# Kernel tuning notes

Hardware: AMD Instinct MI355X
Metric: run time of the kernel (lower is better)

The kernel has to match this reference:

```python
import jax, jax.numpy as jnp
import numpy as np

B, T, H, D = 2, 2048, 8, 128
HID = H * D          # 1024
K_CONV = 4
EPS = 1e-5


def causal_dwconv(x, w, b):
    # x: [B,T,C], w: [C,K], b: [C]
    # torch Conv1d(groups=C, padding=K-1) followed by [..., :T] == left-padded causal depthwise conv
    K = w.shape[1]
    Tx = x.shape[1]
    xp = jnp.pad(x, ((0, 0), (K - 1, 0), (0, 0)))
    acc = jnp.zeros_like(x)
    for j in range(K):  # tiny fixed loop over kernel taps
        acc = acc + xp[:, j:j + Tx, :] * w[:, j]
    return acc + b


def setup_inputs() -> dict:
    key = jax.random.key(0)
    ks = jax.random.split(key, 16)
    s = 0.02
    inp = {
        'x':   jax.random.normal(ks[0], (B, T, HID), jnp.float32),
        'Wq':  s * jax.random.normal(ks[1], (HID, H * D), jnp.float32),
        'Wk':  s * jax.random.normal(ks[2], (HID, H * D), jnp.float32),
        'Wv':  s * jax.random.normal(ks[3], (HID, H * D), jnp.float32),
        'Wa':  s * jax.random.normal(ks[4], (HID, H * D), jnp.float32),
        'ba':  jnp.zeros((H * D,), jnp.float32),
        'Wb':  s * jax.random.normal(ks[5], (HID, H), jnp.float32),
        'bb':  jnp.zeros((H,), jnp.float32),
        'Wg':  s * jax.random.normal(ks[6], (HID, H * D), jnp.float32),
        'Wo':  s * jax.random.normal(ks[7], (H * D, HID), jnp.float32),
        'cqw': s * jax.random.normal(ks[8], (H * D, K_CONV), jnp.float32),
        'cqb': jnp.zeros((H * D,), jnp.float32),
        'ckw': s * jax.random.normal(ks[9], (H * D, K_CONV), jnp.float32),
        'ckb': jnp.zeros((H * D,), jnp.float32),
        'cvw': s * jax.random.normal(ks[10], (H * D, K_CONV), jnp.float32),
        'cvb': jnp.zeros((H * D,), jnp.float32),
        'ln_g': jnp.ones((D,), jnp.float32),
        'ln_b': jnp.zeros((D,), jnp.float32),
    }
    return inp


def reference(x, Wq, Wk, Wv, Wa, ba, Wb, bb, Wg, Wo,
              cqw, cqb, ckw, ckb, cvw, cvb, ln_g, ln_b):
    Bx, Tx, _ = x.shape
    q = x @ Wq
    k = x @ Wk
    v = x @ Wv
    q = jax.nn.silu(causal_dwconv(q, cqw, cqb))
    k = jax.nn.silu(causal_dwconv(k, ckw, ckb))
    v = jax.nn.silu(causal_dwconv(v, cvw, cvb))
    q = q.reshape(Bx, Tx, H, D)
    k = k.reshape(Bx, Tx, H, D) * (D ** -0.5)   # k scaled by head_dim_qk**-0.5
    v = v.reshape(Bx, Tx, H, D)
    a = jax.nn.sigmoid(x @ Wa + ba).reshape(Bx, Tx, H, D)
    beta = jax.nn.sigmoid(x @ Wb + bb)           # [B,T,H]

    # delta-rule recurrent scan; state S: [B,H,Dv,Dk]
    def step(S, inp):
        q_t, k_t, v_t, a_t, b_t = inp            # [B,H,D] / beta [B,H]
        delta = jnp.einsum('bhvk,bhk->bhv', S, k_t)
        err = delta - v_t
        S = a_t[..., None] * S - (b_t[..., None] * err)[..., None] * k_t[:, :, None, :]
        o_t = jnp.einsum('bhvk,bhk->bhv', S, q_t)
        return S, o_t

    tfirst = lambda z: jnp.moveaxis(z, 1, 0)     # [B,T,...] -> [T,B,...]
    S0 = jnp.zeros((Bx, H, D, D), x.dtype)
    _, o = jax.lax.scan(step, S0, (tfirst(q), tfirst(k), tfirst(v), tfirst(a), tfirst(beta)))
    o = jnp.moveaxis(o, 0, 1)                    # [B,T,H,D]

    # LayerNorm over head_dim_v
    mu = o.mean(-1, keepdims=True)
    var = ((o - mu) ** 2).mean(-1, keepdims=True)
    o = (o - mu) * jax.lax.rsqrt(var + EPS) * ln_g + ln_b

    g = jax.nn.sigmoid(x @ Wg).reshape(Bx, Tx, H, D)
    o = (o * g).reshape(Bx, Tx, H * D)
    return o @ Wo
```

## Files before the change

kernel.cpp:

```cpp
#include <hip/hip_runtime.h>
#include <hip/hip_bf16.h>
#include <cstdint>
#include <cstddef>

#define BATCH 2
#define TLEN  2048
#define NHEAD 8
#define HD    128
#define HIDN  1024
#define MTOT  4096
#define MAT_ELEMS 1048576
#define XELEMS 4194304

typedef _Float16 f16;
typedef _Float16 f16x2 __attribute__((ext_vector_type(2)));
typedef _Float16 f16x8 __attribute__((ext_vector_type(8)));
typedef float    f32x4 __attribute__((ext_vector_type(4)));

__device__ __forceinline__ float sigmoidf_(float v) { return 1.0f / (1.0f + __expf(-v)); }

__device__ __forceinline__ float fdot2_(f16x2 a, f16x2 b, float c)
{
#if __has_builtin(__builtin_amdgcn_fdot2)
    return __builtin_amdgcn_fdot2(a, b, c, false);
#else
    return fmaf((float)a.x, (float)b.x, fmaf((float)a.y, (float)b.y, c));
#endif
}

__global__ __launch_bounds__(256) void convert_x_kernel(const float* __restrict__ x,
                                                        f16* __restrict__ x16)
{
    int i = (blockIdx.x * 256 + threadIdx.x) * 4;
    float4 v = *(const float4*)(x + i);
    union { f16 h[4]; uint2 u; } pk;
    pk.h[0] = (f16)v.x; pk.h[1] = (f16)v.y; pk.h[2] = (f16)v.z; pk.h[3] = (f16)v.w;
    *(uint2*)(x16 + i) = pk.u;
}

__global__ __launch_bounds__(256) void transpose_convert_kernel(
    const float* __restrict__ Wq, const float* __restrict__ Wk, const float* __restrict__ Wv,
    const float* __restrict__ Wa, const float* __restrict__ Wg, const float* __restrict__ Wo,
    f16* __restrict__ WT)
{
    __shared__ float tile[32][33];
    int mat = blockIdx.z;
    const float* W = (mat == 0) ? Wq : (mat == 1) ? Wk : (mat == 2) ? Wv
                   : (mat == 3) ? Wa : (mat == 4) ? Wg : Wo;
    int k0 = blockIdx.y * 32, n0 = blockIdx.x * 32;
    int tr = threadIdx.x >> 3;
    int tc = (threadIdx.x & 7) * 4;
    float4 vin = *(const float4*)(W + (size_t)(k0 + tr) * HIDN + n0 + tc);
    tile[tr][tc + 0] = vin.x; tile[tr][tc + 1] = vin.y;
    tile[tr][tc + 2] = vin.z; tile[tr][tc + 3] = vin.w;
    __syncthreads();
    f16* dst = WT + (size_t)(mat * HIDN + n0 + tr) * HIDN + k0 + tc;
    union { f16 h[4]; uint2 u; } pk;
    pk.h[0] = (f16)tile[tc + 0][tr]; pk.h[1] = (f16)tile[tc + 1][tr];
    pk.h[2] = (f16)tile[tc + 2][tr]; pk.h[3] = (f16)tile[tc + 3][tr];
    *(uint2*)dst = pk.u;
}

template <int MODE>
__global__ __launch_bounds__(256) void gemm_f16(
    const f16* __restrict__ A, const f16* __restrict__ BT,
    float* __restrict__ out_f32,
    f16* __restrict__ qkv_hat, float* __restrict__ a_buf, f16* __restrict__ g16,
    const float* __restrict__ ba)
{
    __shared__ __align__(16) f16 As[128][40];
    __shared__ __align__(16) f16 Bs[128][40];
    int m0 = blockIdx.y * 128;
    int n0 = blockIdx.x * 128;
    int tid = threadIdx.x;
    int w = tid >> 6, lane = tid & 63;
    int L16 = lane & 15, quad = lane >> 4;
    int wm = (w >> 1) * 64, wn = (w & 1) * 64;

    f32x4 acc[4][4];
#pragma unroll
    for (int i = 0; i < 4; ++i)
#pragma unroll
        for (int j = 0; j < 4; ++j) acc[i][j] = (f32x4){0.f, 0.f, 0.f, 0.f};

    int ldr = tid >> 2;
    int ldc = (tid & 3) * 8;

    for (int k0 = 0; k0 < 1024; k0 += 32) {
        uint4 a0 = *(const uint4*)(A + (size_t)(m0 + ldr) * HIDN + k0 + ldc);
        uint4 a1 = *(const uint4*)(A + (size_t)(m0 + ldr + 64) * HIDN + k0 + ldc);
        uint4 b0 = *(const uint4*)(BT + (size_t)(n0 + ldr) * HIDN + k0 + ldc);
        uint4 b1 = *(const uint4*)(BT + (size_t)(n0 + ldr + 64) * HIDN + k0 + ldc);
        __syncthreads();
        *(uint4*)(&As[ldr][ldc]) = a0;
        *(uint4*)(&As[ldr + 64][ldc]) = a1;
        *(uint4*)(&Bs[ldr][ldc]) = b0;
        *(uint4*)(&Bs[ldr + 64][ldc]) = b1;
        __syncthreads();
        f16x8 af[4], bf[4];
#pragma unroll
        for (int i = 0; i < 4; ++i) {
            af[i] = *(const f16x8*)(&As[wm + i * 16 + L16][quad * 8]);
            bf[i] = *(const f16x8*)(&Bs[wn + i * 16 + L16][quad * 8]);
        }
#pragma unroll
        for (int i = 0; i < 4; ++i)
#pragma unroll
            for (int j = 0; j < 4; ++j)
                acc[i][j] = __builtin_amdgcn_mfma_f32_16x16x32_f16(af[i], bf[j], acc[i][j], 0, 0, 0);
    }

#pragma unroll
    for (int i = 0; i < 4; ++i) {
#pragma unroll
        for (int j = 0; j < 4; ++j) {
            f32x4 c = acc[i][j];
            int mbase = m0 + wm + i * 16 + quad * 4;
            int n = n0 + wn + j * 16 + L16;
            if (MODE == 1) {
#pragma unroll
                for (int r = 0; r < 4; ++r)
                    out_f32[(size_t)(mbase + r) * HIDN + n] = c[r];
            } else {
                int mat = n >> 10;
                int nn = n & 1023;
                if (mat < 3) {
#pragma unroll
                    for (int r = 0; r < 4; ++r)
                        qkv_hat[(size_t)mat * XELEMS + (size_t)(mbase + r) * HIDN + nn] = (f16)c[r];
                } else if (mat == 3) {
                    float bav = ba[nn];
#pragma unroll
                    for (int r = 0; r < 4; ++r)
                        a_buf[(size_t)(mbase + r) * HIDN + nn] = sigmoidf_(c[r] + bav);
                } else {
#pragma unroll
                    for (int r = 0; r < 4; ++r)
                        g16[(size_t)(mbase + r) * HIDN + nn] = (f16)sigmoidf_(c[r]);
                }
            }
        }
    }
}

__global__ __launch_bounds__(256) void beta_kernel(const float* __restrict__ x,
                                                   const float* __restrict__ Wb,
                                                   const float* __restrict__ bb,
                                                   float* __restrict__ beta_buf)
{
    int row = blockIdx.x;
    int h = threadIdx.x >> 5, lane = threadIdx.x & 31;
    const float* xr = x + (size_t)row * HIDN;
    float part = 0.f;
    for (int i = lane; i < HIDN; i += 32)
        part += xr[i] * Wb[i * NHEAD + h];
#pragma unroll
    for (int m = 1; m <= 16; m <<= 1) part += __shfl_xor(part, m);
    if (lane == 0)
        beta_buf[(size_t)row * NHEAD + h] = sigmoidf_(part + bb[h]);
}

__global__ __launch_bounds__(256) void conv_silu_kernel(
    const f16* __restrict__ qkv_hat,
    const float* __restrict__ cqw, const float* __restrict__ cqb,
    const float* __restrict__ ckw, const float* __restrict__ ckb,
    const float* __restrict__ cvw, const float* __restrict__ cvb,
    f16* __restrict__ qkv16)
{
    int z = blockIdx.y;
    int row = blockIdx.x;
    int tloc = row & (TLEN - 1);
    int c4 = threadIdx.x * 4;
    const f16* src = qkv_hat + (size_t)z * XELEMS;
    const float* w  = (z == 0) ? cqw : (z == 1) ? ckw : cvw;
    const float* bi = (z == 0) ? cqb : (z == 1) ? ckb : cvb;

    float xv[4][4];
#pragma unroll
    for (int j = 0; j < 4; ++j) {
        int tt = tloc - 3 + j;
        if (tt >= 0) {
            const f16* p = src + (size_t)(row - 3 + j) * HIDN + c4;
            xv[j][0] = (float)p[0]; xv[j][1] = (float)p[1];
            xv[j][2] = (float)p[2]; xv[j][3] = (float)p[3];
        } else {
            xv[j][0] = xv[j][1] = xv[j][2] = xv[j][3] = 0.f;
        }
    }
    float scale = (z == 1) ? 0.08838834764831845f : 1.0f;
    union { f16 h[4]; uint2 u; } pk;
#pragma unroll
    for (int cc = 0; cc < 4; ++cc) {
        float4 wc = *(const float4*)(w + (size_t)(c4 + cc) * 4);
        float acc = bi[c4 + cc] + wc.x * xv[0][cc] + wc.y * xv[1][cc]
                                 + wc.z * xv[2][cc] + wc.w * xv[3][cc];
        pk.h[cc] = (f16)(acc * sigmoidf_(acc) * scale);
    }
    *(uint2*)(qkv16 + (size_t)z * XELEMS + (size_t)row * HIDN + c4) = pk.u;
}

#define SCAN_C 32
#define SSC  1024.0f
#define ISSC 0.0009765625f

__global__ __launch_bounds__(64) void scan_kernel(
    const f16* __restrict__ q16, const f16* __restrict__ k16, const f16* __restrict__ v16,
    const float* __restrict__ a_buf, const float* __restrict__ beta_buf,
    float* __restrict__ o_buf)
{
    __shared__ __align__(16) float Sp[16 * 132];
    __shared__ __align__(16) f16   Sp16[16 * 136];
    __shared__ __align__(16) f16   Ks[32 * 136];
    __shared__ __align__(16) f16   Gf[32 * 40];
    __shared__ __align__(16) f16   Qf[32 * 40];
    __shared__ __align__(16) float skv[16 * 34];
    __shared__ __align__(16) float sqv[16 * 34];
    __shared__ __align__(16) float avb[16 * 68];
    __shared__ __align__(16) float Bts[32];
    __shared__ __align__(16) f16   c16s[16 * 40];
    __shared__ __align__(16) float PCs[16];

    int bh = blockIdx.x;
    int b = bh >> 3, h = bh & 7;
    int v0 = blockIdx.y * 16;
    int lane = threadIdx.x;
    int L16 = lane & 15, quad = lane >> 4;
    int vl = lane >> 2, li = lane & 3;
    int t_av = lane >> 1, halfsel = lane & 1;
    const size_t rowbase = (size_t)(b * TLEN) * HIDN + h * HD;

    f16x8 kf[2][4], qf[2][4];
    float4 ar0, ar1; uint4 vr; float betr = 0.f;

    auto prefetch = [&](int t0) {
#pragma unroll
        for (int nt = 0; nt < 2; ++nt)
#pragma unroll
            for (int kk = 0; kk < 4; ++kk) {
                size_t g = rowbase + (size_t)(t0 + nt * 16 + L16) * HIDN + kk * 32 + quad * 8;
                kf[nt][kk] = *(const f16x8*)(k16 + g);
                qf[nt][kk] = *(const f16x8*)(q16 + g);
            }
        size_t ga = rowbase + (size_t)(t0 + t_av) * HIDN + v0 + halfsel * 8;
        ar0 = *(const float4*)(a_buf + ga);
        ar1 = *(const float4*)(a_buf + ga + 4);
        vr  = *(const uint4*)(v16 + ga);
        betr = beta_buf[((size_t)(b * TLEN) + t0 + t_av) * NHEAD + h];
    };

    auto stage = [&]() {
#pragma unroll
        for (int nt = 0; nt < 2; ++nt)
#pragma unroll
            for (int kk = 0; kk < 4; ++kk)
                *(f16x8*)(&Ks[(nt * 16 + L16) * 136 + kk * 32 + quad * 8]) = kf[nt][kk];
        const f16* vh = (const f16*)&vr;
        const float* aa0 = (const float*)&ar0;
        const float* aa1 = (const float*)&ar1;
#pragma unroll
        for (int e = 0; e < 4; ++e) {
            float2 w; w.x = aa0[e]; w.y = betr * (float)vh[e];
            *(float2*)(&avb[(halfsel * 8 + e) * 68 + 2 * t_av]) = w;
        }
#pragma unroll
        for (int e = 0; e < 4; ++e) {
            float2 w; w.x = aa1[e]; w.y = betr * (float)vh[4 + e];
            *(float2*)(&avb[(halfsel * 8 + 4 + e) * 68 + 2 * t_av]) = w;
        }
        if (halfsel == 0) Bts[t_av] = betr;
    };

    auto computeMM = [&]() {
        f32x4 accG[2][2], accKQ[2][2], accK[2], accQ[2];
#pragma unroll
        for (int i = 0; i < 2; ++i) {
            accK[i] = (f32x4){0, 0, 0, 0}; accQ[i] = (f32x4){0, 0, 0, 0};
#pragma unroll
            for (int j = 0; j < 2; ++j) { accG[i][j] = (f32x4){0, 0, 0, 0}; accKQ[i][j] = (f32x4){0, 0, 0, 0}; }
        }
#pragma unroll
        for (int kk = 0; kk < 4; ++kk) {
            f16x8 sf = *(const f16x8*)(&Sp16[L16 * 136 + kk * 32 + quad * 8]);
#pragma unroll
            for (int nt = 0; nt < 2; ++nt) {
                accK[nt] = __builtin_amdgcn_mfma_f32_16x16x32_f16(sf, kf[nt][kk], accK[nt], 0, 0, 0);
                accQ[nt] = __builtin_amdgcn_mfma_f32_16x16x32_f16(sf, qf[nt][kk], accQ[nt], 0, 0, 0);
#pragma unroll
                for (int mt = 0; mt < 2; ++mt) {
                    accG[mt][nt]  = __builtin_amdgcn_mfma_f32_16x16x32_f16(kf[mt][kk], kf[nt][kk], accG[mt][nt], 0, 0, 0);
                    accKQ[mt][nt] = __builtin_amdgcn_mfma_f32_16x16x32_f16(kf[mt][kk], qf[nt][kk], accKQ[mt][nt], 0, 0, 0);
                }
            }
        }
#pragma unroll
        for (int nt = 0; nt < 2; ++nt) {
            int t = nt * 16 + L16;
#pragma unroll
            for (int mt = 0; mt < 2; ++mt) {
                union { f16 e[4]; uint2 u2; } pg, pq;
#pragma unroll
                for (int r = 0; r < 4; ++r) {
                    pg.e[r] = (f16)accG[mt][nt][r];
                    pq.e[r] = (f16)accKQ[mt][nt][r];
                }
                *(uint2*)(&Gf[t * 40 + mt * 16 + quad * 4]) = pg.u2;
                *(uint2*)(&Qf[t * 40 + mt * 16 + quad * 4]) = pq.u2;
            }
#pragma unroll
            for (int r = 0; r < 4; ++r) {
                skv[(quad * 4 + r) * 34 + t] = accK[nt][r];
                sqv[(quad * 4 + r) * 34 + t] = accQ[nt][r];
            }
        }
    };

    prefetch(0);
    for (int i = lane; i < 16 * 132; i += 64) Sp[i] = 0.f;
    for (int i = lane; i < 16 * 136; i += 64) Sp16[i] = (f16)0.f;

    const size_t obase = rowbase + v0 + vl;
    const int NCH = TLEN / SCAN_C;

    for (int ch = 0; ch < NCH; ++ch) {
        int t0 = ch * SCAN_C;
        stage();
        computeMM();

        f16x8 bu[8];
#pragma unroll
        for (int kt = 0; kt < 8; ++kt)
#pragma unroll
            for (int j = 0; j < 8; ++j)
                bu[kt][j] = Ks[(quad * 8 + j) * 136 + kt * 16 + L16];

        if (ch < NCH - 1) prefetch(t0 + SCAN_C);

        {
            f16x2 c0, c1, c2, c3;
            c0.x = (f16)0.f; c0.y = (f16)0.f; c1 = c0; c2 = c0; c3 = c0;
            float P = 1.f;
            union RowU { uint4 u4; f16x2 p[4]; };
#pragma unroll
            for (int t = 0; t < SCAN_C; t += 2) {
                RowU g0u, g1u, h0u, h1u;
                g0u.u4 = *(const uint4*)(&Gf[t * 40 + li * 8]);
                g1u.u4 = *(const uint4*)(&Gf[(t + 1) * 40 + li * 8]);
                h0u.u4 = *(const uint4*)(&Qf[t * 40 + li * 8]);
                h1u.u4 = *(const uint4*)(&Qf[(t + 1) * 40 + li * 8]);
                float2 skp = *(const float2*)(&skv[vl * 34 + t]);
                float2 sqp = *(const float2*)(&sqv[vl * 34 + t]);
                float4 ab4 = *(const float4*)(&avb[vl * 68 + 2 * t]);
                float2 btp = *(const float2*)(&Bts[t]);
                float kq00 = (float)Qf[t * 40 + t];
                f16x2 dq  = *(const f16x2*)(&Qf[(t + 1) * 40 + t]);
                float g01 = (float)Gf[(t + 1) * 40 + t];

                float pG  = fdot2_(c0, g0u.p[0], fdot2_(c1, g0u.p[1], 0.f))
                          + fdot2_(c2, g0u.p[2], fdot2_(c3, g0u.p[3], 0.f));
                float pG1 = fdot2_(c0, g1u.p[0], fdot2_(c1, g1u.p[1], 0.f))
                          + fdot2_(c2, g1u.p[2], fdot2_(c3, g1u.p[3], 0.f));
                float pO  = fdot2_(c0, h0u.p[0], fdot2_(c1, h0u.p[1], 0.f))
                          + fdot2_(c2, h0u.p[2], fdot2_(c3, h0u.p[3], 0.f));
                float pO1 = fdot2_(c0, h1u.p[0], fdot2_(c1, h1u.p[1], 0.f))
                          + fdot2_(c2, h1u.p[2], fdot2_(c3, h1u.p[3], 0.f));
                int tmp;
                tmp = __builtin_amdgcn_update_dpp(0, __float_as_int(pG),  0xB1, 0xF, 0xF, true); pG  += __int_as_float(tmp);
                tmp = __builtin_amdgcn_update_dpp(0, __float_as_int(pG1), 0xB1, 0xF, 0xF, true); pG1 += __int_as_float(tmp);
                tmp = __builtin_amdgcn_update_dpp(0, __float_as_int(pO),  0xB1, 0xF, 0xF, true); pO  += __int_as_float(tmp);
                tmp = __builtin_amdgcn_update_dpp(0, __float_as_int(pO1), 0xB1, 0xF, 0xF, true); pO1 += __int_as_float(tmp);
                tmp = __builtin_amdgcn_update_dpp(0, __float_as_int(pG),  0x4E, 0xF, 0xF, true); pG  += __int_as_float(tmp);
                tmp = __builtin_amdgcn_update_dpp(0, __float_as_int(pG1), 0x4E, 0xF, 0xF, true); pG1 += __int_as_float(tmp);
                tmp = __builtin_amdgcn_update_dpp(0, __float_as_int(pO),  0x4E, 0xF, 0xF, true); pO  += __int_as_float(tmp);
                tmp = __builtin_amdgcn_update_dpp(0, __float_as_int(pO1), 0x4E, 0xF, 0xF, true); pO1 += __int_as_float(tmp);

                float a0 = ab4.x, bv0 = ab4.y, a1 = ab4.z, bv1 = ab4.w;
                float bt0 = btp.x, bt1 = btp.y;
                float sk0 = skp.x * ISSC, sk1 = skp.y * ISSC;
                float sq0 = sqp.x * ISSC, sq1 = sqp.y * ISSC;
                float kq01 = (float)dq.x, kq11 = (float)dq.y;

                float x0 = fmaf(P, sk0, pG);
                float u0 = fmaf(-bt0, x0, bv0);
                float P0 = P * a0;
                float o0 = fmaf(a0, pO, u0 * kq00);
                o0 = fmaf(P0, sq0, o0);
                float accGv = fmaf(a0, pG1, u0 * g01);
                float x1 = fmaf(P0, sk1, accGv);
                float u1 = fmaf(-bt1, x1, bv1);
                float P1 = P0 * a1;
                float accOv = fmaf(a0, pO1, u0 * kq01);
                float o1 = fmaf(a1, accOv, u1 * kq11);
                o1 = fmaf(P1, sq1, o1);

                float aa = a0 * a1;
                f16 aah = (f16)aa;
                f16x2 aa2; aa2.x = aah; aa2.y = aah;
                c0 *= aa2; c1 *= aa2; c2 *= aa2; c3 *= aa2;
                if (li == (t >> 3)) {
                    f16x2 un; un.x = (f16)(u0 * a1); un.y = (f16)u1;
                    int p = (t & 7) >> 1;
                    if (p == 0) c0 = un; else if (p == 1) c1 = un;
                    else if (p == 2) c2 = un; else c3 = un;
                }
                P = P1;
                if (li == 0) {
                    o_buf[obase + (size_t)(t0 + t) * HIDN]     = o0;
                    o_buf[obase + (size_t)(t0 + t + 1) * HIDN] = o1;
                }
            }
            f16 s16 = (f16)SSC;
            f16x2 ss2; ss2.x = s16; ss2.y = s16;
            union { f16x2 p[4]; uint4 u4; } pc;
            pc.p[0] = c0 * ss2; pc.p[1] = c1 * ss2; pc.p[2] = c2 * ss2; pc.p[3] = c3 * ss2;
            *(uint4*)(&c16s[vl * 40 + li * 8]) = pc.u4;
            if (li == 0) PCs[vl] = P;
        }

        if (ch < NCH - 1) {
            f16x8 ca = *(const f16x8*)(&c16s[L16 * 40 + quad * 8]);
            float pc = PCs[L16];
#pragma unroll
            for (int kt = 0; kt < 8; ++kt) {
                f32x4 d = __builtin_amdgcn_mfma_f32_16x16x32_f16(bu[kt], ca, (f32x4){0, 0, 0, 0}, 0, 0, 0);
                int idx = L16 * 132 + kt * 16 + quad * 4;
                float4 s = *(const float4*)(&Sp[idx]);
                s.x = fmaf(pc, s.x, d[0]);
                s.y = fmaf(pc, s.y, d[1]);
                s.z = fmaf(pc, s.z, d[2]);
                s.w = fmaf(pc, s.w, d[3]);
                *(float4*)(&Sp[idx]) = s;
                union { f16 e[4]; uint2 u2; } ph;
                ph.e[0] = (f16)s.x; ph.e[1] = (f16)s.y;
                ph.e[2] = (f16)s.z; ph.e[3] = (f16)s.w;
                *(uint2*)(&Sp16[L16 * 136 + kt * 16 + quad * 4]) = ph.u2;
            }
        }
    }
}

__global__ __launch_bounds__(256) void ln_gate_kernel(
    const float* __restrict__ o_buf, const f16* __restrict__ g16,
    const float* __restrict__ lng, const float* __restrict__ lnb,
    f16* __restrict__ og16)
{
    int row = blockIdx.x;
    int h = threadIdx.x >> 5, lane = threadIdx.x & 31;
    size_t base = (size_t)row * HIDN + h * HD + lane * 4;
    float4 x = *(const float4*)(o_buf + base);
    float s  = x.x + x.y + x.z + x.w;
    float sq = x.x * x.x + x.y * x.y + x.z * x.z + x.w * x.w;
#pragma unroll
    for (int m = 1; m <= 16; m <<= 1) {
        s  += __shfl_xor(s, m);
        sq += __shfl_xor(sq, m);
    }
    float mu  = s * (1.0f / 128.0f);
    float var = sq * (1.0f / 128.0f) - mu * mu;
    float inv = 1.0f / sqrtf(var + 1e-5f);
    int d = lane * 4;
    const float* xp = (const float*)&x;
    union { f16 h4[4]; uint2 u; } pk;
#pragma unroll
    for (int j = 0; j < 4; ++j) {
        float on = (xp[j] - mu) * inv * lng[d + j] + lnb[d + j];
        pk.h4[j] = (f16)(on * (float)g16[base + j]);
    }
    *(uint2*)(og16 + base) = pk.u;
}

extern "C" void kernel_launch(void* const* d_in, const int* in_sizes, int n_in,
                              void* d_out, int out_size, void* d_ws, size_t ws_size,
                              hipStream_t stream)
{
    (void)in_sizes; (void)n_in; (void)out_size; (void)ws_size;
    const float* x   = (const float*)d_in[0];
    const float* Wq  = (const float*)d_in[1];
    const float* Wk  = (const float*)d_in[2];
    const float* Wv  = (const float*)d_in[3];
    const float* Wa  = (const float*)d_in[4];
    const float* ba  = (const float*)d_in[5];
    const float* Wb  = (const float*)d_in[6];
    const float* bb  = (const float*)d_in[7];
    const float* Wg  = (const float*)d_in[8];
    const float* Wo  = (const float*)d_in[9];
    const float* cqw = (const float*)d_in[10];
    const float* cqb = (const float*)d_in[11];
    const float* ckw = (const float*)d_in[12];
    const float* ckb = (const float*)d_in[13];
    const float* cvw = (const float*)d_in[14];
    const float* cvb = (const float*)d_in[15];
    const float* lng = (const float*)d_in[16];
    const float* lnb = (const float*)d_in[17];
    float* out = (float*)d_out;

    char* ws = (char*)d_ws;
    f16*   x16      = (f16*)(ws + 0);
    f16*   WT       = (f16*)(ws + 8388608);
    f16*   qkvh     = (f16*)(ws + 20971520);
    f16*   qkv16    = (f16*)(ws + 46137344);
    float* a_buf    = (float*)(ws + 96468992);
    f16*   g16      = (f16*)(ws + 113246208);
    float* beta_buf = (float*)(ws + 121634816);
    float* o_buf    = (float*)(ws + 121765888);
    f16*   og16     = (f16*)(ws + 138543104);

    convert_x_kernel<<<dim3(4096), dim3(256), 0, stream>>>(x, x16);
    transpose_convert_kernel<<<dim3(32, 32, 6), dim3(256), 0, stream>>>(Wq, Wk, Wv, Wa, Wg, Wo, WT);
    gemm_f16<0><<<dim3(40, 32), dim3(256), 0, stream>>>(x16, WT, nullptr, qkvh, a_buf, g16, ba);
    beta_kernel<<<dim3(4096), dim3(256), 0, stream>>>(x, Wb, bb, beta_buf);
    conv_silu_kernel<<<dim3(4096, 3), dim3(256), 0, stream>>>(qkvh, cqw, cqb, ckw, ckb, cvw, cvb, qkv16);
    scan_kernel<<<dim3(16, 8), dim3(64), 0, stream>>>(
        qkv16, qkv16 + XELEMS, qkv16 + 2 * (size_t)XELEMS, a_buf, beta_buf, o_buf);
    ln_gate_kernel<<<dim3(4096), dim3(256), 0, stream>>>(o_buf, g16, lng, lnb, og16);
    gemm_f16<1><<<dim3(8, 32), dim3(256), 0, stream>>>(og16, WT + 5 * (size_t)MAT_ELEMS, out,
                                                       nullptr, nullptr, nullptr, nullptr);
}
```

Before: 614.2 us.

## Precompute chunk Gram matrices in a parallel kernel and warp-specialize the scan

A new gram_kernel computes the per-chunk K·K^T and K·Q^T Gram matrices, plus cross-chunk Gram terms and a transposed K, in parallel across all chunks, and writes them to the workspace. The scan becomes a two-wave block: one wave prefetches those matrices, a/beta/v and next-chunk K/Q into double-buffered LDS and runs the state-update and S·K/S·Q MFMAs, while the other wave runs the serial intra-chunk recurrence. This takes Gram work off the serial critical path and overlaps loads and state updates with the recurrence. In exchange it adds extra global traffic, an extra launch, per-chunk block barriers and a more intricate cross-chunk correction scheme.

```diff
diff --git a/kernel.cpp b/kernel.cpp
--- a/kernel.cpp
+++ b/kernel.cpp
@@ -11,6 +11,10 @@
 #define MTOT  4096
 #define MAT_ELEMS 1048576
 #define XELEMS 4194304
+#define SCAN_C 32
+#define NCH    64
+#define SSC  1024.0f
+#define ISSC 0.0009765625f
 
 typedef _Float16 f16;
 typedef _Float16 f16x2 __attribute__((ext_vector_type(2)));
@@ -199,241 +203,390 @@
     *(uint2*)(qkv16 + (size_t)z * XELEMS + (size_t)row * HIDN + c4) = pk.u;
 }
 
-#define SCAN_C 32
-#define SSC  1024.0f
-#define ISSC 0.0009765625f
-
-__global__ __launch_bounds__(64) void scan_kernel(
+__global__ __launch_bounds__(64) void gram_kernel(
+    const f16* __restrict__ q16, const f16* __restrict__ k16,
+    f16* __restrict__ G_g, f16* __restrict__ KQ_g,
+    f16* __restrict__ Gx_g, f16* __restrict__ Qx_g, f16* __restrict__ KT_g)
+{
+    int ch = blockIdx.x;
+    int bh = blockIdx.y;
+    int b = bh >> 3, h = bh & 7;
+    int lane = threadIdx.x;
+    int L16 = lane & 15, quad = lane >> 4;
+    size_t rowbase = (size_t)(b * TLEN) * HIDN + h * HD;
+    int t0 = ch * SCAN_C;
+    bool hasNext = (ch + 1 < NCH);
+
+    union ZU { uint4 u; f16x8 v; };
+    ZU zz; zz.u = (uint4){0, 0, 0, 0};
+
+    f16x8 kc[2][4], qc[2][4], kn[2][4], qn[2][4];
+#pragma unroll
+    for (int nt = 0; nt < 2; ++nt)
+#pragma unroll
+        for (int kk = 0; kk < 4; ++kk) {
+            size_t g = rowbase + (size_t)(t0 + nt * 16 + L16) * HIDN + kk * 32 + quad * 8;
+            kc[nt][kk] = *(const f16x8*)(k16 + g);
+            qc[nt][kk] = *(const f16x8*)(q16 + g);
+            if (hasNext) {
+                kn[nt][kk] = *(const f16x8*)(k16 + g + (size_t)SCAN_C * HIDN);
+                qn[nt][kk] = *(const f16x8*)(q16 + g + (size_t)SCAN_C * HIDN);
+            } else {
+                kn[nt][kk] = zz.v; qn[nt][kk] = zz.v;
+            }
+        }
+
+    f32x4 aG[2][2], aKQ[2][2], aGx[2][2], aQx[2][2];
+#pragma unroll
+    for (int i = 0; i < 2; ++i)
+#pragma unroll
+        for (int j = 0; j < 2; ++j) {
+            aG[i][j] = (f32x4){0, 0, 0, 0}; aKQ[i][j] = (f32x4){0, 0, 0, 0};
+            aGx[i][j] = (f32x4){0, 0, 0, 0}; aQx[i][j] = (f32x4){0, 0, 0, 0};
+        }
+#pragma unroll
+    for (int kk = 0; kk < 4; ++kk)
+#pragma unroll
+        for (int mt = 0; mt < 2; ++mt)
+#pragma unroll
+            for (int nt = 0; nt < 2; ++nt) {
+                aG[mt][nt]  = __builtin_amdgcn_mfma_f32_16x16x32_f16(kc[mt][kk], kc[nt][kk], aG[mt][nt], 0, 0, 0);
+                aKQ[mt][nt] = __builtin_amdgcn_mfma_f32_16x16x32_f16(kc[mt][kk], qc[nt][kk], aKQ[mt][nt], 0, 0, 0);
+                aGx[mt][nt] = __builtin_amdgcn_mfma_f32_16x16x32_f16(kc[mt][kk], kn[nt][kk], aGx[mt][nt], 0, 0, 0);
+                aQx[mt][nt] = __builtin_amdgcn_mfma_f32_16x16x32_f16(kc[mt][kk], qn[nt][kk], aQx[mt][nt], 0, 0, 0);
+            }
+
+    size_t gb = ((size_t)bh * NCH + ch) * 1024;
+#pragma unroll
+    for (int nt = 0; nt < 2; ++nt) {
+        int t = nt * 16 + L16;
+#pragma unroll
+        for (int mt = 0; mt < 2; ++mt) {
+            union { f16 e[4]; uint2 u2; } pg, pq, px, py;
+#pragma unroll
+            for (int r = 0; r < 4; ++r) {
+                pg.e[r] = (f16)aG[mt][nt][r];
+                pq.e[r] = (f16)aKQ[mt][nt][r];
+                px.e[r] = (f16)aGx[mt][nt][r];
+                py.e[r] = (f16)aQx[mt][nt][r];
+            }
+            *(uint2*)(G_g  + gb + t * 32 + mt * 16 + quad * 4) = pg.u2;
+            *(uint2*)(KQ_g + gb + t * 32 + mt * 16 + quad * 4) = pq.u2;
+            *(uint2*)(Gx_g + gb + t * 32 + mt * 16 + quad * 4) = px.u2;
+            *(uint2*)(Qx_g + gb + t * 32 + mt * 16 + quad * 4) = py.u2;
+        }
+    }
+    size_t kb = ((size_t)bh * NCH + ch) * 4096;
+#pragma unroll
+    for (int nt = 0; nt < 2; ++nt) {
+        int t = nt * 16 + L16;
+#pragma unroll
+        for (int kk = 0; kk < 4; ++kk)
+#pragma unroll
+            for (int j = 0; j < 8; ++j) {
+                int k = kk * 32 + quad * 8 + j;
+                KT_g[kb + (size_t)k * 32 + t] = kc[nt][kk][j];
+            }
+    }
+}
+
+__global__ __launch_bounds__(128) void scan2_kernel(
     const f16* __restrict__ q16, const f16* __restrict__ k16, const f16* __restrict__ v16,
     const float* __restrict__ a_buf, const float* __restrict__ beta_buf,
+    const f16* __restrict__ G_g, const f16* __restrict__ KQ_g,
+    const f16* __restrict__ Gx_g, const f16* __restrict__ Qx_g, const f16* __restrict__ KT_g,
     float* __restrict__ o_buf)
 {
     __shared__ __align__(16) float Sp[16 * 132];
     __shared__ __align__(16) f16   Sp16[16 * 136];
-    __shared__ __align__(16) f16   Ks[32 * 136];
-    __shared__ __align__(16) f16   Gf[32 * 40];
-    __shared__ __align__(16) f16   Qf[32 * 40];
-    __shared__ __align__(16) float skv[16 * 34];
-    __shared__ __align__(16) float sqv[16 * 34];
-    __shared__ __align__(16) float avb[16 * 68];
-    __shared__ __align__(16) float Bts[32];
-    __shared__ __align__(16) f16   c16s[16 * 40];
-    __shared__ __align__(16) float PCs[16];
-
-    int bh = blockIdx.x;
-    int b = bh >> 3, h = bh & 7;
-    int v0 = blockIdx.y * 16;
-    int lane = threadIdx.x;
-    int L16 = lane & 15, quad = lane >> 4;
-    int vl = lane >> 2, li = lane & 3;
-    int t_av = lane >> 1, halfsel = lane & 1;
+    __shared__ __align__(16) f16   KT_lds[128 * 32];
+    __shared__ __align__(16) f16   G_lds[2][1024];
+    __shared__ __align__(16) f16   Q_lds[2][1024];
+    __shared__ __align__(16) f16   Gx_lds[2][1024];
+    __shared__ __align__(16) f16   Qx_lds[2][1024];
+    __shared__ __align__(16) float skv[2][16 * 34];
+    __shared__ __align__(16) float sqv[2][16 * 34];
+    __shared__ __align__(16) float avb[2][16 * 68];
+    __shared__ __align__(16) float Bts[2][32];
+    __shared__ __align__(16) f16   c16s[2][16 * 40];
+    __shared__ __align__(16) float PCs[2][16];
+
+    const int tid = threadIdx.x;
+    const int wid = tid >> 6;
+    const int lane = tid & 63;
+    const int L16 = lane & 15, quad = lane >> 4;
+    const int vl = lane >> 2, li = lane & 3;
+    const int t_av = lane >> 1, halfsel = lane & 1;
+
+    const int bh = blockIdx.x;
+    const int b = bh >> 3, h = bh & 7;
+    const int v0 = blockIdx.y * 16;
     const size_t rowbase = (size_t)(b * TLEN) * HIDN + h * HD;
-
-    f16x8 kf[2][4], qf[2][4];
-    float4 ar0, ar1; uint4 vr; float betr = 0.f;
-
-    auto prefetch = [&](int t0) {
-#pragma unroll
-        for (int nt = 0; nt < 2; ++nt)
-#pragma unroll
-            for (int kk = 0; kk < 4; ++kk) {
-                size_t g = rowbase + (size_t)(t0 + nt * 16 + L16) * HIDN + kk * 32 + quad * 8;
-                kf[nt][kk] = *(const f16x8*)(k16 + g);
-                qf[nt][kk] = *(const f16x8*)(q16 + g);
-            }
-        size_t ga = rowbase + (size_t)(t0 + t_av) * HIDN + v0 + halfsel * 8;
-        ar0 = *(const float4*)(a_buf + ga);
-        ar1 = *(const float4*)(a_buf + ga + 4);
-        vr  = *(const uint4*)(v16 + ga);
-        betr = beta_buf[((size_t)(b * TLEN) + t0 + t_av) * NHEAD + h];
-    };
-
-    auto stage = [&]() {
-#pragma unroll
-        for (int nt = 0; nt < 2; ++nt)
-#pragma unroll
-            for (int kk = 0; kk < 4; ++kk)
-                *(f16x8*)(&Ks[(nt * 16 + L16) * 136 + kk * 32 + quad * 8]) = kf[nt][kk];
-        const f16* vh = (const f16*)&vr;
-        const float* aa0 = (const float*)&ar0;
-        const float* aa1 = (const float*)&ar1;
-#pragma unroll
-        for (int e = 0; e < 4; ++e) {
-            float2 w; w.x = aa0[e]; w.y = betr * (float)vh[e];
-            *(float2*)(&avb[(halfsel * 8 + e) * 68 + 2 * t_av]) = w;
-        }
-#pragma unroll
-        for (int e = 0; e < 4; ++e) {
-            float2 w; w.x = aa1[e]; w.y = betr * (float)vh[4 + e];
-            *(float2*)(&avb[(halfsel * 8 + 4 + e) * 68 + 2 * t_av]) = w;
-        }
-        if (halfsel == 0) Bts[t_av] = betr;
-    };
-
-    auto computeMM = [&]() {
-        f32x4 accG[2][2], accKQ[2][2], accK[2], accQ[2];
-#pragma unroll
-        for (int i = 0; i < 2; ++i) {
-            accK[i] = (f32x4){0, 0, 0, 0}; accQ[i] = (f32x4){0, 0, 0, 0};
-#pragma unroll
-            for (int j = 0; j < 2; ++j) { accG[i][j] = (f32x4){0, 0, 0, 0}; accKQ[i][j] = (f32x4){0, 0, 0, 0}; }
-        }
-#pragma unroll
-        for (int kk = 0; kk < 4; ++kk) {
-            f16x8 sf = *(const f16x8*)(&Sp16[L16 * 136 + kk * 32 + quad * 8]);
-#pragma unroll
-            for (int nt = 0; nt < 2; ++nt) {
-                accK[nt] = __builtin_amdgcn_mfma_f32_16x16x32_f16(sf, kf[nt][kk], accK[nt], 0, 0, 0);
-                accQ[nt] = __builtin_amdgcn_mfma_f32_16x16x32_f16(sf, qf[nt][kk], accQ[nt], 0, 0, 0);
-#pragma unroll
-                for (int mt = 0; mt < 2; ++mt) {
-                    accG[mt][nt]  = __builtin_amdgcn_mfma_f32_16x16x32_f16(kf[mt][kk], kf[nt][kk], accG[mt][nt], 0, 0, 0);
-                    accKQ[mt][nt] = __builtin_amdgcn_mfma_f32_16x16x32_f16(kf[mt][kk], qf[nt][kk], accKQ[mt][nt], 0, 0, 0);
-                }
-            }
-        }
-#pragma unroll
-        for (int nt = 0; nt < 2; ++nt) {
-            int t = nt * 16 + L16;
-#pragma unroll
-            for (int mt = 0; mt < 2; ++mt) {
-                union { f16 e[4]; uint2 u2; } pg, pq;
+    const size_t gmatbase = (size_t)bh * NCH;
+
+    {
+        for (int i = tid; i < 16 * 132; i += 128) Sp[i] = 0.f;
+        uint32_t* z;
+        z = (uint32_t*)Sp16;    for (int i = tid; i < 16 * 136 / 2; i += 128) z[i] = 0u;
+        z = (uint32_t*)KT_lds;  for (int i = tid; i < 128 * 32 / 2;  i += 128) z[i] = 0u;
+        z = (uint32_t*)G_lds;   for (int i = tid; i < 1024;          i += 128) z[i] = 0u;
+        z = (uint32_t*)Q_lds;   for (int i = tid; i < 1024;          i += 128) z[i] = 0u;
+        z = (uint32_t*)Gx_lds;  for (int i = tid; i < 1024;          i += 128) z[i] = 0u;
+        z = (uint32_t*)Qx_lds;  for (int i = tid; i < 1024;          i += 128) z[i] = 0u;
+        z = (uint32_t*)skv;     for (int i = tid; i < 2 * 16 * 34;   i += 128) z[i] = 0u;
+        z = (uint32_t*)sqv;     for (int i = tid; i < 2 * 16 * 34;   i += 128) z[i] = 0u;
+        z = (uint32_t*)avb;     for (int i = tid; i < 2 * 16 * 68;   i += 128) z[i] = 0u;
+        z = (uint32_t*)Bts;     for (int i = tid; i < 2 * 32;        i += 128) z[i] = 0u;
+        z = (uint32_t*)c16s;    for (int i = tid; i < 2 * 16 * 40 / 2; i += 128) z[i] = 0u;
+        z = (uint32_t*)PCs;     for (int i = tid; i < 2 * 16;        i += 128) z[i] = 0u;
+    }
+    __syncthreads();
+
+    if (wid == 1) {
+        f16x8 kf[2][4], qf[2][4];
+
+        {
+            size_t gb0 = gmatbase * 1024;
+            *(uint4*)(&G_lds[0][lane * 16])     = *(const uint4*)(G_g  + gb0 + lane * 16);
+            *(uint4*)(&G_lds[0][lane * 16 + 8]) = *(const uint4*)(G_g  + gb0 + lane * 16 + 8);
+            *(uint4*)(&Q_lds[0][lane * 16])     = *(const uint4*)(KQ_g + gb0 + lane * 16);
+            *(uint4*)(&Q_lds[0][lane * 16 + 8]) = *(const uint4*)(KQ_g + gb0 + lane * 16 + 8);
+            size_t ga = rowbase + (size_t)t_av * HIDN + v0 + halfsel * 8;
+            float4 ar0 = *(const float4*)(a_buf + ga);
+            float4 ar1 = *(const float4*)(a_buf + ga + 4);
+            uint4  vr  = *(const uint4*)(v16 + ga);
+            float betr = beta_buf[((size_t)(b * TLEN) + t_av) * NHEAD + h];
+            const f16* vh = (const f16*)&vr;
+            const float* aa0 = (const float*)&ar0;
+            const float* aa1 = (const float*)&ar1;
+#pragma unroll
+            for (int e = 0; e < 4; ++e) {
+                float2 wv; wv.x = aa0[e]; wv.y = betr * (float)vh[e];
+                *(float2*)(&avb[0][(halfsel * 8 + e) * 68 + 2 * t_av]) = wv;
+                float2 wu; wu.x = aa1[e]; wu.y = betr * (float)vh[4 + e];
+                *(float2*)(&avb[0][(halfsel * 8 + 4 + e) * 68 + 2 * t_av]) = wu;
+            }
+            if (halfsel == 0) Bts[0][t_av] = betr;
+        }
+        __syncthreads();
+
+        for (int ch = 0; ch < NCH; ++ch) {
+            const int p = ch & 1;
+            const int np = p ^ 1;
+            const bool haveNext = (ch + 1 < NCH);
+
+            if (ch >= 1 && ch <= NCH - 2) {
+                f16x8 ca = *(const f16x8*)(&c16s[np][L16 * 40 + quad * 8]);
+                float pc = PCs[np][L16];
+#pragma unroll
+                for (int kt = 0; kt < 8; ++kt) {
+                    f16x8 bu = *(const f16x8*)(&KT_lds[(kt * 16 + L16) * 32 + quad * 8]);
+                    f32x4 d = __builtin_amdgcn_mfma_f32_16x16x32_f16(bu, ca, (f32x4){0, 0, 0, 0}, 0, 0, 0);
+                    int idx = L16 * 132 + kt * 16 + quad * 4;
+                    float4 s = *(const float4*)(&Sp[idx]);
+                    s.x = fmaf(pc, s.x, d[0]);
+                    s.y = fmaf(pc, s.y, d[1]);
+                    s.z = fmaf(pc, s.z, d[2]);
+                    s.w = fmaf(pc, s.w, d[3]);
+                    *(float4*)(&Sp[idx]) = s;
+                    union { f16 e[4]; uint2 u2; } ph;
+                    ph.e[0] = (f16)s.x; ph.e[1] = (f16)s.y;
+                    ph.e[2] = (f16)s.z; ph.e[3] = (f16)s.w;
+                    *(uint2*)(&Sp16[L16 * 136 + kt * 16 + quad * 4]) = ph.u2;
+                }
+                f32x4 accK[2], accQ[2];
+                accK[0] = (f32x4){0, 0, 0, 0}; accK[1] = (f32x4){0, 0, 0, 0};
+                accQ[0] = (f32x4){0, 0, 0, 0}; accQ[1] = (f32x4){0, 0, 0, 0};
+#pragma unroll
+                for (int kk = 0; kk < 4; ++kk) {
+                    f16x8 sf = *(const f16x8*)(&Sp16[L16 * 136 + kk * 32 + quad * 8]);
+#pragma unroll
+                    for (int nt = 0; nt < 2; ++nt) {
+                        accK[nt] = __builtin_amdgcn_mfma_f32_16x16x32_f16(sf, kf[nt][kk], accK[nt], 0, 0, 0);
+                        accQ[nt] = __builtin_amdgcn_mfma_f32_16x16x32_f16(sf, qf[nt][kk], accQ[nt], 0, 0, 0);
+                    }
+                }
+#pragma unroll
+                for (int nt = 0; nt < 2; ++nt) {
+                    int t = nt * 16 + L16;
+#pragma unroll
+                    for (int r = 0; r < 4; ++r) {
+                        skv[np][(quad * 4 + r) * 34 + t] = accK[nt][r];
+                        sqv[np][(quad * 4 + r) * 34 + t] = accQ[nt][r];
+                    }
+                }
+            }
+
+            if (haveNext) {
+                size_t gbn = (gmatbase + ch + 1) * 1024;
+                size_t gbc = (gmatbase + ch) * 1024;
+                uint4 tg0 = *(const uint4*)(G_g  + gbn + lane * 16);
+                uint4 tg1 = *(const uint4*)(G_g  + gbn + lane * 16 + 8);
+                uint4 tq0 = *(const uint4*)(KQ_g + gbn + lane * 16);
+                uint4 tq1 = *(const uint4*)(KQ_g + gbn + lane * 16 + 8);
+                uint4 tx0 = *(const uint4*)(Gx_g + gbc + lane * 16);
+                uint4 tx1 = *(const uint4*)(Gx_g + gbc + lane * 16 + 8);
+                uint4 ty0 = *(const uint4*)(Qx_g + gbc + lane * 16);
+                uint4 ty1 = *(const uint4*)(Qx_g + gbc + lane * 16 + 8);
+                *(uint4*)(&G_lds[np][lane * 16])      = tg0;
+                *(uint4*)(&G_lds[np][lane * 16 + 8])  = tg1;
+                *(uint4*)(&Q_lds[np][lane * 16])      = tq0;
+                *(uint4*)(&Q_lds[np][lane * 16 + 8])  = tq1;
+                *(uint4*)(&Gx_lds[np][lane * 16])     = tx0;
+                *(uint4*)(&Gx_lds[np][lane * 16 + 8]) = tx1;
+                *(uint4*)(&Qx_lds[np][lane * 16])     = ty0;
+                *(uint4*)(&Qx_lds[np][lane * 16 + 8]) = ty1;
+                size_t kb = (gmatbase + ch) * 4096;
+#pragma unroll
+                for (int i = 0; i < 8; ++i) {
+                    uint4 tk = *(const uint4*)(KT_g + kb + lane * 8 + (size_t)i * 512);
+                    *(uint4*)(&KT_lds[lane * 8 + i * 512]) = tk;
+                }
+                int tn = (ch + 1) * SCAN_C;
+                size_t ga = rowbase + (size_t)(tn + t_av) * HIDN + v0 + halfsel * 8;
+                float4 ar0 = *(const float4*)(a_buf + ga);
+                float4 ar1 = *(const float4*)(a_buf + ga + 4);
+                uint4  vr  = *(const uint4*)(v16 + ga);
+                float betr = beta_buf[((size_t)(b * TLEN) + tn + t_av) * NHEAD + h];
+                const f16* vh = (const f16*)&vr;
+                const float* aa0 = (const float*)&ar0;
+                const float* aa1 = (const float*)&ar1;
+#pragma unroll
+                for (int e = 0; e < 4; ++e) {
+                    float2 wv; wv.x = aa0[e]; wv.y = betr * (float)vh[e];
+                    *(float2*)(&avb[np][(halfsel * 8 + e) * 68 + 2 * t_av]) = wv;
+                    float2 wu; wu.x = aa1[e]; wu.y = betr * (float)vh[4 + e];
+                    *(float2*)(&avb[np][(halfsel * 8 + 4 + e) * 68 + 2 * t_av]) = wu;
+                }
+                if (halfsel == 0) Bts[np][t_av] = betr;
+            }
+
+            if (ch <= NCH - 3) {
+                int tp = (ch + 2) * SCAN_C;
+#pragma unroll
+                for (int nt = 0; nt < 2; ++nt)
+#pragma unroll
+                    for (int kk = 0; kk < 4; ++kk) {
+                        size_t g = rowbase + (size_t)(tp + nt * 16 + L16) * HIDN + kk * 32 + quad * 8;
+                        kf[nt][kk] = *(const f16x8*)(k16 + g);
+                        qf[nt][kk] = *(const f16x8*)(q16 + g);
+                    }
+            }
+            __syncthreads();
+        }
+    } else {
+        __syncthreads();
+        const size_t obase = rowbase + v0 + vl;
+
+        for (int ch = 0; ch < NCH; ++ch) {
+            const int p = ch & 1;
+            const int np = p ^ 1;
+            const int t0 = ch * SCAN_C;
+
+            {
+                f16x8 caf = *(const f16x8*)(&c16s[np][L16 * 40 + quad * 8]);
+                f32x4 fK[2], fQ[2];
+#pragma unroll
+                for (int nt = 0; nt < 2; ++nt) {
+                    f16x8 bx = *(const f16x8*)(&Gx_lds[p][(nt * 16 + L16) * 32 + quad * 8]);
+                    f16x8 by = *(const f16x8*)(&Qx_lds[p][(nt * 16 + L16) * 32 + quad * 8]);
+                    fK[nt] = __builtin_amdgcn_mfma_f32_16x16x32_f16(caf, bx, (f32x4){0, 0, 0, 0}, 0, 0, 0);
+                    fQ[nt] = __builtin_amdgcn_mfma_f32_16x16x32_f16(caf, by, (f32x4){0, 0, 0, 0}, 0, 0, 0);
+                }
 #pragma unroll
                 for (int r = 0; r < 4; ++r) {
-                    pg.e[r] = (f16)accG[mt][nt][r];
-                    pq.e[r] = (f16)accKQ[mt][nt][r];
-                }
-                *(uint2*)(&Gf[t * 40 + mt * 16 + quad * 4]) = pg.u2;
-                *(uint2*)(&Qf[t * 40 + mt * 16 + quad * 4]) = pq.u2;
-            }
-#pragma unroll
-            for (int r = 0; r < 4; ++r) {
-                skv[(quad * 4 + r) * 34 + t] = accK[nt][r];
-                sqv[(quad * 4 + r) * 34 + t] = accQ[nt][r];
-            }
-        }
-    };
-
-    prefetch(0);
-    for (int i = lane; i < 16 * 132; i += 64) Sp[i] = 0.f;
-    for (int i = lane; i < 16 * 136; i += 64) Sp16[i] = (f16)0.f;
-
-    const size_t obase = rowbase + v0 + vl;
-    const int NCH = TLEN / SCAN_C;
-
-    for (int ch = 0; ch < NCH; ++ch) {
-        int t0 = ch * SCAN_C;
-        stage();
-        computeMM();
-
-        f16x8 bu[8];
-#pragma unroll
-        for (int kt = 0; kt < 8; ++kt)
-#pragma unroll
-            for (int j = 0; j < 8; ++j)
-                bu[kt][j] = Ks[(quad * 8 + j) * 136 + kt * 16 + L16];
-
-        if (ch < NCH - 1) prefetch(t0 + SCAN_C);
-
-        {
-            f16x2 c0, c1, c2, c3;
-            c0.x = (f16)0.f; c0.y = (f16)0.f; c1 = c0; c2 = c0; c3 = c0;
-            float P = 1.f;
-            union RowU { uint4 u4; f16x2 p[4]; };
-#pragma unroll
-            for (int t = 0; t < SCAN_C; t += 2) {
-                RowU g0u, g1u, h0u, h1u;
-                g0u.u4 = *(const uint4*)(&Gf[t * 40 + li * 8]);
-                g1u.u4 = *(const uint4*)(&Gf[(t + 1) * 40 + li * 8]);
-                h0u.u4 = *(const uint4*)(&Qf[t * 40 + li * 8]);
-                h1u.u4 = *(const uint4*)(&Qf[(t + 1) * 40 + li * 8]);
-                float2 skp = *(const float2*)(&skv[vl * 34 + t]);
-                float2 sqp = *(const float2*)(&sqv[vl * 34 + t]);
-                float4 ab4 = *(const float4*)(&avb[vl * 68 + 2 * t]);
-                float2 btp = *(const float2*)(&Bts[t]);
-                float kq00 = (float)Qf[t * 40 + t];
-                f16x2 dq  = *(const f16x2*)(&Qf[(t + 1) * 40 + t]);
-                float g01 = (float)Gf[(t + 1) * 40 + t];
-
-                float pG  = fdot2_(c0, g0u.p[0], fdot2_(c1, g0u.p[1], 0.f))
-                          + fdot2_(c2, g0u.p[2], fdot2_(c3, g0u.p[3], 0.f));
-                float pG1 = fdot2_(c0, g1u.p[0], fdot2_(c1, g1u.p[1], 0.f))
-                          + fdot2_(c2, g1u.p[2], fdot2_(c3, g1u.p[3], 0.f));
-                float pO  = fdot2_(c0, h0u.p[0], fdot2_(c1, h0u.p[1], 0.f))
-                          + fdot2_(c2, h0u.p[2], fdot2_(c3, h0u.p[3], 0.f));
-                float pO1 = fdot2_(c0, h1u.p[0], fdot2_(c1, h1u.p[1], 0.f))
-                          + fdot2_(c2, h1u.p[2], fdot2_(c3, h1u.p[3], 0.f));
-                int tmp;
-                tmp = __builtin_amdgcn_update_dpp(0, __float_as_int(pG),  0xB1, 0xF, 0xF, true); pG  += __int_as_float(tmp);
-                tmp = __builtin_amdgcn_update_dpp(0, __float_as_int(pG1), 0xB1, 0xF, 0xF, true); pG1 += __int_as_float(tmp);
-                tmp = __builtin_amdgcn_update_dpp(0, __float_as_int(pO),  0xB1, 0xF, 0xF, true); pO  += __int_as_float(tmp);
-                tmp = __builtin_amdgcn_update_dpp(0, __float_as_int(pO1), 0xB1, 0xF, 0xF, true); pO1 += __int_as_float(tmp);
-                tmp = __builtin_amdgcn_update_dpp(0, __float_as_int(pG),  0x4E, 0xF, 0xF, true); pG  += __int_as_float(tmp);
-                tmp = __builtin_amdgcn_update_dpp(0, __float_as_int(pG1), 0x4E, 0xF, 0xF, true); pG1 += __int_as_float(tmp);
-                tmp = __builtin_amdgcn_update_dpp(0, __float_as_int(pO),  0x4E, 0xF, 0xF, true); pO  += __int_as_float(tmp);
-                tmp = __builtin_amdgcn_update_dpp(0, __float_as_int(pO1), 0x4E, 0xF, 0xF, true); pO1 += __int_as_float(tmp);
-
-                float a0 = ab4.x, bv0 = ab4.y, a1 = ab4.z, bv1 = ab4.w;
-                float bt0 = btp.x, bt1 = btp.y;
-                float sk0 = skp.x * ISSC, sk1 = skp.y * ISSC;
-                float sq0 = sqp.x * ISSC, sq1 = sqp.y * ISSC;
-                float kq01 = (float)dq.x, kq11 = (float)dq.y;
-
-                float x0 = fmaf(P, sk0, pG);
-                float u0 = fmaf(-bt0, x0, bv0);
-                float P0 = P * a0;
-                float o0 = fmaf(a0, pO, u0 * kq00);
-                o0 = fmaf(P0, sq0, o0);
-                float accGv = fmaf(a0, pG1, u0 * g01);
-                float x1 = fmaf(P0, sk1, accGv);
-                float u1 = fmaf(-bt1, x1, bv1);
-                float P1 = P0 * a1;
-                float accOv = fmaf(a0, pO1, u0 * kq01);
-                float o1 = fmaf(a1, accOv, u1 * kq11);
-                o1 = fmaf(P1, sq1, o1);
-
-                float aa = a0 * a1;
-                f16 aah = (f16)aa;
-                f16x2 aa2; aa2.x = aah; aa2.y = aah;
-                c0 *= aa2; c1 *= aa2; c2 *= aa2; c3 *= aa2;
-                if (li == (t >> 3)) {
-                    f16x2 un; un.x = (f16)(u0 * a1); un.y = (f16)u1;
-                    int p = (t & 7) >> 1;
-                    if (p == 0) c0 = un; else if (p == 1) c1 = un;
-                    else if (p == 2) c2 = un; else c3 = un;
-                }
-                P = P1;
-                if (li == 0) {
-                    o_buf[obase + (size_t)(t0 + t) * HIDN]     = o0;
-                    o_buf[obase + (size_t)(t0 + t + 1) * HIDN] = o1;
-                }
-            }
-            f16 s16 = (f16)SSC;
-            f16x2 ss2; ss2.x = s16; ss2.y = s16;
-            union { f16x2 p[4]; uint4 u4; } pc;
-            pc.p[0] = c0 * ss2; pc.p[1] = c1 * ss2; pc.p[2] = c2 * ss2; pc.p[3] = c3 * ss2;
-            *(uint4*)(&c16s[vl * 40 + li * 8]) = pc.u4;
-            if (li == 0) PCs[vl] = P;
-        }
-
-        if (ch < NCH - 1) {
-            f16x8 ca = *(const f16x8*)(&c16s[L16 * 40 + quad * 8]);
-            float pc = PCs[L16];
-#pragma unroll
-            for (int kt = 0; kt < 8; ++kt) {
-                f32x4 d = __builtin_amdgcn_mfma_f32_16x16x32_f16(bu[kt], ca, (f32x4){0, 0, 0, 0}, 0, 0, 0);
-                int idx = L16 * 132 + kt * 16 + quad * 4;
-                float4 s = *(const float4*)(&Sp[idx]);
-                s.x = fmaf(pc, s.x, d[0]);
-                s.y = fmaf(pc, s.y, d[1]);
-                s.z = fmaf(pc, s.z, d[2]);
-                s.w = fmaf(pc, s.w, d[3]);
-                *(float4*)(&Sp[idx]) = s;
-                union { f16 e[4]; uint2 u2; } ph;
-                ph.e[0] = (f16)s.x; ph.e[1] = (f16)s.y;
-                ph.e[2] = (f16)s.z; ph.e[3] = (f16)s.w;
-                *(uint2*)(&Sp16[L16 * 136 + kt * 16 + quad * 4]) = ph.u2;
-            }
+                    int vv = quad * 4 + r;
+                    float Pv = PCs[np][vv];
+#pragma unroll
+                    for (int nt = 0; nt < 2; ++nt) {
+                        int t = nt * 16 + L16;
+                        skv[p][vv * 34 + t] = fmaf(Pv, skv[p][vv * 34 + t], fK[nt][r]);
+                        sqv[p][vv * 34 + t] = fmaf(Pv, sqv[p][vv * 34 + t], fQ[nt][r]);
+                    }
+                }
+            }
+
+            {
+                f16x2 c0, c1, c2, c3;
+                c0.x = (f16)0.f; c0.y = (f16)0.f; c1 = c0; c2 = c0; c3 = c0;
+                float P = 1.f;
+                union RowU { uint4 u4; f16x2 h2[4]; };
+#pragma unroll
+                for (int t = 0; t < SCAN_C; t += 2) {
+                    RowU g0u, g1u, h0u, h1u;
+                    g0u.u4 = *(const uint4*)(&G_lds[p][t * 32 + li * 8]);
+                    g1u.u4 = *(const uint4*)(&G_lds[p][(t + 1) * 32 + li * 8]);
+                    h0u.u4 = *(const uint4*)(&Q_lds[p][t * 32 + li * 8]);
+                    h1u.u4 = *(const uint4*)(&Q_lds[p][(t + 1) * 32 + li * 8]);
+                    float2 skp = *(const float2*)(&skv[p][vl * 34 + t]);
+                    float2 sqp = *(const float2*)(&sqv[p][vl * 34 + t]);
+                    float4 ab4 = *(const float4*)(&avb[p][vl * 68 + 2 * t]);
+                    float2 btp = *(const float2*)(&Bts[p][t]);
+                    float kq00 = (float)Q_lds[p][t * 32 + t];
+                    f16x2 dq  = *(const f16x2*)(&Q_lds[p][(t + 1) * 32 + t]);
+                    float g01 = (float)G_lds[p][(t + 1) * 32 + t];
+
+                    float pG  = fdot2_(c0, g0u.h2[0], fdot2_(c1, g0u.h2[1], 0.f))
+                              + fdot2_(c2, g0u.h2[2], fdot2_(c3, g0u.h2[3], 0.f));
+                    float pG1 = fdot2_(c0, g1u.h2[0], fdot2_(c1, g1u.h2[1], 0.f))
+                              + fdot2_(c2, g1u.h2[2], fdot2_(c3, g1u.h2[3], 0.f));
+                    float pO  = fdot2_(c0, h0u.h2[0], fdot2_(c1, h0u.h2[1], 0.f))
+                              + fdot2_(c2, h0u.h2[2], fdot2_(c3, h0u.h2[3], 0.f));
+                    float pO1 = fdot2_(c0, h1u.h2[0], fdot2_(c1, h1u.h2[1], 0.f))
+                              + fdot2_(c2, h1u.h2[2], fdot2_(c3, h1u.h2[3], 0.f));
+                    int tmp;
+                    tmp = __builtin_amdgcn_update_dpp(0, __float_as_int(pG),  0xB1, 0xF, 0xF, true); pG  += __int_as_float(tmp);
+                    tmp = __builtin_amdgcn_update_dpp(0, __float_as_int(pG1), 0xB1, 0xF, 0xF, true); pG1 += __int_as_float(tmp);
+                    tmp = __builtin_amdgcn_update_dpp(0, __float_as_int(pO),  0xB1, 0xF, 0xF, true); pO  += __int_as_float(tmp);
+                    tmp = __builtin_amdgcn_update_dpp(0, __float_as_int(pO1), 0xB1, 0xF, 0xF, true); pO1 += __int_as_float(tmp);
+                    tmp = __builtin_amdgcn_update_dpp(0, __float_as_int(pG),  0x4E, 0xF, 0xF, true); pG  += __int_as_float(tmp);
+                    tmp = __builtin_amdgcn_update_dpp(0, __float_as_int(pG1), 0x4E, 0xF, 0xF, true); pG1 += __int_as_float(tmp);
+                    tmp = __builtin_amdgcn_update_dpp(0, __float_as_int(pO),  0x4E, 0xF, 0xF, true); pO  += __int_as_float(tmp);
+                    tmp = __builtin_amdgcn_update_dpp(0, __float_as_int(pO1), 0x4E, 0xF, 0xF, true); pO1 += __int_as_float(tmp);
+
+                    float a0 = ab4.x, bv0 = ab4.y, a1 = ab4.z, bv1 = ab4.w;
+                    float bt0 = btp.x, bt1 = btp.y;
+                    float sk0 = skp.x * ISSC, sk1 = skp.y * ISSC;
+                    float sq0 = sqp.x * ISSC, sq1 = sqp.y * ISSC;
+                    float kq01 = (float)dq.x, kq11 = (float)dq.y;
+
+                    float x0 = fmaf(P, sk0, pG);
+                    float u0 = fmaf(-bt0, x0, bv0);
+                    float P0 = P * a0;
+                    float o0 = fmaf(a0, pO, u0 * kq00);
+                    o0 = fmaf(P0, sq0, o0);
+                    float accGv = fmaf(a0, pG1, u0 * g01);
+                    float x1 = fmaf(P0, sk1, accGv);
+                    float u1 = fmaf(-bt1, x1, bv1);
+                    float P1 = P0 * a1;
+                    float accOv = fmaf(a0, pO1, u0 * kq01);
+                    float o1 = fmaf(a1, accOv, u1 * kq11);
+                    o1 = fmaf(P1, sq1, o1);
+
+                    float aa = a0 * a1;
+                    f16 aah = (f16)aa;
+                    f16x2 aa2; aa2.x = aah; aa2.y = aah;
+                    c0 *= aa2; c1 *= aa2; c2 *= aa2; c3 *= aa2;
+                    if (li == (t >> 3)) {
+                        f16x2 un; un.x = (f16)(u0 * a1); un.y = (f16)u1;
+                        int sel = (t & 7) >> 1;
+                        if (sel == 0) c0 = un; else if (sel == 1) c1 = un;
+                        else if (sel == 2) c2 = un; else c3 = un;
+                    }
+                    P = P1;
+                    if (li == 0) {
+                        o_buf[obase + (size_t)(t0 + t) * HIDN]     = o0;
+                        o_buf[obase + (size_t)(t0 + t + 1) * HIDN] = o1;
+                    }
+                }
+                f16 s16 = (f16)SSC;
+                f16x2 ss2; ss2.x = s16; ss2.y = s16;
+                union { f16x2 h2[4]; uint4 u4; } pc;
+                pc.h2[0] = c0 * ss2; pc.h2[1] = c1 * ss2; pc.h2[2] = c2 * ss2; pc.h2[3] = c3 * ss2;
+                *(uint4*)(&c16s[p][vl * 40 + li * 8]) = pc.u4;
+                if (li == 0) PCs[p][vl] = P;
+            }
+            __syncthreads();
         }
     }
 }
@@ -504,13 +657,22 @@
     float* o_buf    = (float*)(ws + 121765888);
     f16*   og16     = (f16*)(ws + 138543104);
 
+    f16* G_g  = qkvh;
+    f16* KQ_g = qkvh + 1048576;
+    f16* Gx_g = qkvh + 2097152;
+    f16* Qx_g = qkvh + 3145728;
+    f16* KT_g = qkvh + 4194304;
+
     convert_x_kernel<<<dim3(4096), dim3(256), 0, stream>>>(x, x16);
     transpose_convert_kernel<<<dim3(32, 32, 6), dim3(256), 0, stream>>>(Wq, Wk, Wv, Wa, Wg, Wo, WT);
     gemm_f16<0><<<dim3(40, 32), dim3(256), 0, stream>>>(x16, WT, nullptr, qkvh, a_buf, g16, ba);
     beta_kernel<<<dim3(4096), dim3(256), 0, stream>>>(x, Wb, bb, beta_buf);
     conv_silu_kernel<<<dim3(4096, 3), dim3(256), 0, stream>>>(qkvh, cqw, cqb, ckw, ckb, cvw, cvb, qkv16);
-    scan_kernel<<<dim3(16, 8), dim3(64), 0, stream>>>(
-        qkv16, qkv16 + XELEMS, qkv16 + 2 * (size_t)XELEMS, a_buf, beta_buf, o_buf);
+    gram_kernel<<<dim3(NCH, 16), dim3(64), 0, stream>>>(
+        qkv16, qkv16 + XELEMS, G_g, KQ_g, Gx_g, Qx_g, KT_g);
+    scan2_kernel<<<dim3(16, 8), dim3(128), 0, stream>>>(
+        qkv16, qkv16 + XELEMS, qkv16 + 2 * (size_t)XELEMS, a_buf, beta_buf,
+        G_g, KQ_g, Gx_g, Qx_g, KT_g, o_buf);
     ln_gate_kernel<<<dim3(4096), dim3(256), 0, stream>>>(o_buf, g16, lng, lnb, og16);
     gemm_f16<1><<<dim3(8, 32), dim3(256), 0, stream>>>(og16, WT + 5 * (size_t)MAT_ELEMS, out,
                                                        nullptr, nullptr, nullptr, nullptr);
```

Measured after the change: 572.3 us. -6.8%, faster.
